# Kernel optimization log

Hardware: AMD Instinct MI355X
Metric: run time of the kernel (lower is better)

## Reference

```python
import jax, jax.numpy as jnp
import numpy as np

B, CIN, H, W = 32, 16, 32, 128
COUT = 128


def _run_direction(x_hwbc, p):
    # x_hwbc: (H, W, B, CIN); scan order is raster (top-to-bottom, left-to-right).
    # Predecessors: dim0 = cell above (previous row), dim1 = cell to the left.
    xi = jnp.einsum('hwbc,oc->hwbo', x_hwbc, p['w_ii'])
    xf = jnp.einsum('hwbc,oc->hwbo', x_hwbc, p['w_if'])
    xg = jnp.einsum('hwbc,oc->hwbo', x_hwbc, p['w_ig'])
    xo = jnp.einsum('hwbc,oc->hwbo', x_hwbc, p['w_io'])
    Wdim, Bdim = x_hwbc.shape[1], x_hwbc.shape[2]
    O = p['w_hi'].shape[0]
    ws0, ws1 = p['ws'][0], p['ws'][1]

    def branch(xi_, xf_, xg_, xo_, c, h):
        i = jax.nn.sigmoid(xi_ + h @ p['w_hi'].T + p['b_i'])
        f = jax.nn.sigmoid(xf_ + h @ p['w_hf'].T + p['b_f'])
        g = jnp.tanh(xg_ + h @ p['w_hg'].T + p['b_g'])
        o = jax.nn.sigmoid(xo_ + h @ p['w_ho'].T + p['b_o'])
        cn = f * c + i * g
        return cn, o * jnp.tanh(cn)

    def col_step(carry, inp):
        c_left, h_left = carry                      # (B, O)
        xi_, xf_, xg_, xo_, c_top, h_top = inp      # each (B, O)
        c0, h0 = branch(xi_, xf_, xg_, xo_, c_top, h_top)   # vertical predecessor
        c1, h1 = branch(xi_, xf_, xg_, xo_, c_left, h_left) # horizontal predecessor
        ct = ws0 * c0 + ws1 * c1 + p['bias']
        ht = ws0 * h0 + ws1 * h1 + p['bias']
        return (ct, ht), (ct, ht)

    def row_step(carry, row):
        c_top, h_top = carry                        # (W, B, O)
        xi_r, xf_r, xg_r, xo_r = row
        z = jnp.zeros((Bdim, O), xi_r.dtype)
        _, (c_row, h_row) = jax.lax.scan(col_step, (z, z), (xi_r, xf_r, xg_r, xo_r, c_top, h_top))
        return (c_row, h_row), h_row

    z_row = jnp.zeros((Wdim, Bdim, O), x_hwbc.dtype)
    _, h_all = jax.lax.scan(row_step, (z_row, z_row), (xi, xf, xg, xo))
    return h_all  # (H, W, B, O)


def _forward(x, w_ii, w_hi, b_i, w_if, w_hf, b_f, w_ig, w_hg, b_g,
             w_io, w_ho, b_o, weighted_sum, bias):
    # Four scan directions realized by flipping the grid (lr_tb, rl_tb, lr_bt, rl_bt).
    x_hwbc = jnp.transpose(x, (2, 3, 0, 1))  # (H, W, B, CIN)
    flips = [(False, False), (False, True), (True, False), (True, True)]
    outs = []
    for d, (fy, fx) in enumerate(flips):
        xd = x_hwbc
        if fy:
            xd = xd[::-1]
        if fx:
            xd = xd[:, ::-1]
        p = {'w_ii': w_ii[d], 'w_hi': w_hi[d], 'b_i': b_i[d],
             'w_if': w_if[d], 'w_hf': w_hf[d], 'b_f': b_f[d],
             'w_ig': w_ig[d], 'w_hg': w_hg[d], 'b_g': b_g[d],
             'w_io': w_io[d], 'w_ho': w_ho[d], 'b_o': b_o[d],
             'ws': weighted_sum[d], 'bias': bias[d]}
        h = _run_direction(xd, p)
        if fy:
            h = h[::-1]
        if fx:
            h = h[:, ::-1]
        outs.append(h)
    h4 = jnp.stack(outs)                      # (4, H, W, B, O)
    return jnp.transpose(h4, (0, 4, 3, 1, 2)) # (4, O, B, H, W)


def setup_inputs() -> dict:
    key = jax.random.key(0)
    ks = jax.random.split(key, 16)
    xw = lambda k: jax.random.normal(k, (4, COUT, CIN), jnp.float32) * 0.05
    hw = lambda k: jax.random.normal(k, (4, COUT, COUT), jnp.float32) * 0.05
    bb = lambda k: jax.random.normal(k, (4, COUT), jnp.float32) * 0.05
    return {
        'x': jax.random.normal(ks[0], (B, CIN, H, W), jnp.float32),
        'w_ii': xw(ks[1]), 'w_hi': hw(ks[2]), 'b_i': bb(ks[3]),
        'w_if': xw(ks[4]), 'w_hf': hw(ks[5]), 'b_f': bb(ks[6]),
        'w_ig': xw(ks[7]), 'w_hg': hw(ks[8]), 'b_g': bb(ks[9]),
        'w_io': xw(ks[10]), 'w_ho': hw(ks[11]), 'b_o': bb(ks[12]),
        'weighted_sum': jax.random.uniform(ks[13], (4, 2), jnp.float32),
        'bias': bb(ks[14]),
    }


def reference(x, w_ii, w_hi, b_i, w_if, w_hf, b_f, w_ig, w_hg, b_g,
              w_io, w_ho, b_o, weighted_sum, bias):
    return _forward(x, w_ii, w_hi, b_i, w_if, w_hf, b_f, w_ig, w_hg, b_g,
                    w_io, w_ho, b_o, weighted_sum, bias)
```

## Files before the change

### kernel.cpp

```cpp
#include <hip/hip_runtime.h>

#define Hh 32
#define Ww 128
#define BB 32
#define CC 16
#define OO 128
#define SPIN_CAP (1 << 23)
#define FSTRIDE 32

typedef __attribute__((ext_vector_type(8))) short short8;
typedef __attribute__((ext_vector_type(4))) float f32x4;

__device__ inline short f2bf(float f) {
    unsigned u = __builtin_bit_cast(unsigned, f);
    unsigned r = (u + 0x7FFFu + ((u >> 16) & 1u)) >> 16;
    return (short)r;
}
__device__ inline float bf2f(short s) {
    unsigned u = ((unsigned)(unsigned short)s) << 16;
    return __builtin_bit_cast(float, u);
}
__device__ inline float rcp_(float x) { return __builtin_amdgcn_rcpf(x); }
__device__ inline float sigm(float x) {
    return rcp_(1.f + __builtin_amdgcn_exp2f(-1.442695041f * x));
}
__device__ inline float tanh_(float x) {
    return 1.f - 2.f * rcp_(__builtin_amdgcn_exp2f(2.885390082f * x) + 1.f);
}

__device__ inline unsigned long long aload64(const unsigned long long* p) {
    return __hip_atomic_load(p, __ATOMIC_RELAXED, __HIP_MEMORY_SCOPE_AGENT);
}
__device__ inline void astore64(unsigned long long* p, unsigned long long v) {
    __hip_atomic_store(p, v, __ATOMIC_RELAXED, __HIP_MEMORY_SCOPE_AGENT);
}
__device__ inline void astore16(short* p, short v) {
    __hip_atomic_store(p, v, __ATOMIC_RELAXED, __HIP_MEMORY_SCOPE_AGENT);
}
__device__ inline int aloadI(const int* p) {
    return __hip_atomic_load(p, __ATOMIC_RELAXED, __HIP_MEMORY_SCOPE_AGENT);
}
__device__ inline void astoreI(int* p, int v) {
    __hip_atomic_store(p, v, __ATOMIC_RELAXED, __HIP_MEMORY_SCOPE_AGENT);
}

__global__ void mdlstm_init(const float* __restrict__ x, short* __restrict__ xT,
                            int* __restrict__ flags) {
    int idx = blockIdx.x * 256 + threadIdx.x;
    if (blockIdx.x < 64) flags[idx] = 0;
    int w = idx & 127;
    int h = (idx >> 7) & 31;
    int c = (idx >> 12) & 15;
    int b = idx >> 16;
    float v = x[idx];
    xT[((h * Ww + w) * BB + b) * CC + c] = f2bf(v);
}

__global__ void __launch_bounds__(512, 1) mdlstm_main(
    const short* __restrict__ xT,
    const float* __restrict__ w_ii, const float* __restrict__ w_hi, const float* __restrict__ b_i,
    const float* __restrict__ w_if, const float* __restrict__ w_hf, const float* __restrict__ b_f,
    const float* __restrict__ w_ig, const float* __restrict__ w_hg, const float* __restrict__ b_g,
    const float* __restrict__ w_io, const float* __restrict__ w_ho, const float* __restrict__ b_o,
    const float* __restrict__ wsum, const float* __restrict__ bias,
    short* __restrict__ hring, float* __restrict__ cring,
    int* __restrict__ prog, int* __restrict__ cons,
    float* __restrict__ out, int depth)
{
    const int chain = blockIdx.x & 7;
    const int r     = blockIdx.x >> 3;
    const int d     = chain >> 1;
    const int s     = chain & 1;
    const int b0    = s * 16;
    const bool fy   = (d >= 2);
    const bool fx   = (d & 1);
    const int hh    = fy ? (Hh - 1 - r) : r;

    const int tid  = threadIdx.x;
    const int wv   = tid >> 6;
    const int lane = tid & 63;
    const int lr   = lane & 15;
    const int lh   = lane >> 4;
    const int on   = wv * 16 + lr;

    __shared__ short stage[OO * 256];

    const float* whp[4] = {w_hi, w_hf, w_hg, w_ho};
    const float* wip[4] = {w_ii, w_if, w_ig, w_io};
    short8 whf[4][4];
    short8 wif_[4];
#pragma unroll
    for (int g = 0; g < 4; ++g) {
#pragma unroll
        for (int kt = 0; kt < 4; ++kt) {
            const float* p = whp[g] + ((d * OO + on) * OO + kt * 32 + lh * 8);
            short8 f;
#pragma unroll
            for (int j = 0; j < 8; ++j) f[j] = f2bf(p[j]);
            whf[g][kt] = f;
        }
        short8 fi = (short8)(short)0;
        if (lh < 2) {
            const float* p = wip[g] + ((d * OO + on) * CC + lh * 8);
#pragma unroll
            for (int j = 0; j < 8; ++j) fi[j] = f2bf(p[j]);
        }
        wif_[g] = fi;
    }

    const float bi  = b_i[d * OO + on];
    const float bf_ = b_f[d * OO + on];
    const float bg_ = b_g[d * OO + on];
    const float bo_ = b_o[d * OO + on];
    const float bb_ = bias[d * OO + on];
    const float ws0 = wsum[d * 2 + 0];
    const float ws1 = wsum[d * 2 + 1];

    int* topf      = prog + ((d * 32 + (r - 1)) * 2 + s) * FSTRIDE;
    int* myprog    = prog + ((d * 32 + r) * 2 + s) * FSTRIDE;
    int* mycons    = cons + ((d * 32 + r) * 2 + s) * FSTRIDE;
    int* consnext  = cons + ((d * 32 + (r + 1)) * 2 + s) * FSTRIDE;

    const int rbh_me  = ((d * 32 + r)     * 2 + s) * depth * (16 * OO);
    const int rbh_top = ((d * 32 + (r-1)) * 2 + s) * depth * (16 * OO);
    const int rbc_me  = ((d * 32 + r)     * 2 + s) * depth * (OO * 16);
    const int rbc_top = ((d * 32 + (r-1)) * 2 + s) * depth * (OO * 16);
    const int smask   = depth - 1;

    short8 hLf[4];
#pragma unroll
    for (int kt = 0; kt < 4; ++kt) hLf[kt] = (short8)(short)0;
    float cL[4] = {0.f, 0.f, 0.f, 0.f};

    short8 hTfB[4];
#pragma unroll
    for (int kt = 0; kt < 4; ++kt) hTfB[kt] = (short8)(short)0;
    float cTB[4] = {0.f, 0.f, 0.f, 0.f};

    int top_seen = 0, cons_seen = 0;
    const f32x4 zacc = {0.f, 0.f, 0.f, 0.f};

#pragma unroll 2
    for (int wsc = 0; wsc < Ww; ++wsc) {
        const int ww    = fx ? (Ww - 1 - wsc) : wsc;
        const int slot  = wsc & smask;
        const int wslot = ww & 15;
        const bool evenc = ((wsc & 1) == 0);

        short8 xf = (short8)(short)0;
        if (lh < 2) {
            const short8* p = (const short8*)(xT + ((hh * Ww + ww) * BB + b0 + lr) * CC + lh * 8);
            xf = __builtin_nontemporal_load(p);
        }

        short8 hTf[4];
        float cT[4];
        if (r > 0) {
            if (evenc) {
                const int need = wsc + 2;
                if (top_seen < need) {
                    int spin = 0;
                    while (top_seen < need && spin < SPIN_CAP) {
                        int v = 0;
                        if (lane == 0) v = aloadI(topf);
                        v = __shfl(v, 0, 64);
                        if (v < need) { __builtin_amdgcn_s_sleep(1); ++spin; } else top_seen = v;
                    }
                }
                const short* hb = hring + rbh_top + slot * (16 * OO) + lr * OO;
#pragma unroll
                for (int kt = 0; kt < 4; ++kt) {
                    union { unsigned long long q; short8 v8; } u, u2;
                    u.q = aload64((const unsigned long long*)(hb + kt * 32 + lh * 8));
                    (void)u2;
                    union { unsigned long long q[2]; short8 v; } w;
                    w.q[0] = aload64((const unsigned long long*)(hb + kt * 32 + lh * 8));
                    w.q[1] = aload64((const unsigned long long*)(hb + kt * 32 + lh * 8 + 4));
                    hTf[kt] = w.v;
                }
                const short* hb2 = hb + 16 * OO;
#pragma unroll
                for (int kt = 0; kt < 4; ++kt) {
                    union { unsigned long long q[2]; short8 v; } w;
                    w.q[0] = aload64((const unsigned long long*)(hb2 + kt * 32 + lh * 8));
                    w.q[1] = aload64((const unsigned long long*)(hb2 + kt * 32 + lh * 8 + 4));
                    hTfB[kt] = w.v;
                }
                const unsigned long long* cp =
                    (const unsigned long long*)(cring + rbc_top + slot * (OO * 16) + on * 16 + lh * 4);
                union { unsigned long long q; float f[2]; } c01, c23;
                c01.q = aload64(cp);
                c23.q = aload64(cp + 1);
                cT[0] = c01.f[0]; cT[1] = c01.f[1]; cT[2] = c23.f[0]; cT[3] = c23.f[1];
                const unsigned long long* cpB =
                    (const unsigned long long*)(cring + rbc_top + (slot + 1) * (OO * 16) + on * 16 + lh * 4);
                c01.q = aload64(cpB);
                c23.q = aload64(cpB + 1);
                cTB[0] = c01.f[0]; cTB[1] = c01.f[1]; cTB[2] = c23.f[0]; cTB[3] = c23.f[1];
            } else {
#pragma unroll
                for (int kt = 0; kt < 4; ++kt) hTf[kt] = hTfB[kt];
#pragma unroll
                for (int j = 0; j < 4; ++j) cT[j] = cTB[j];
            }
        } else {
#pragma unroll
            for (int kt = 0; kt < 4; ++kt) hTf[kt] = (short8)(short)0;
#pragma unroll
            for (int j = 0; j < 4; ++j) cT[j] = 0.f;
        }

        f32x4 ax[4], accL[4], accT[4];
#pragma unroll
        for (int g = 0; g < 4; ++g)
            ax[g] = __builtin_amdgcn_mfma_f32_16x16x32_bf16(xf, wif_[g], zacc, 0, 0, 0);
#pragma unroll
        for (int g = 0; g < 4; ++g) {
            f32x4 a = ax[g];
#pragma unroll
            for (int kt = 0; kt < 4; ++kt)
                a = __builtin_amdgcn_mfma_f32_16x16x32_bf16(hLf[kt], whf[g][kt], a, 0, 0, 0);
            accL[g] = a;
        }
#pragma unroll
        for (int g = 0; g < 4; ++g) {
            f32x4 a = ax[g];
#pragma unroll
            for (int kt = 0; kt < 4; ++kt)
                a = __builtin_amdgcn_mfma_f32_16x16x32_bf16(hTf[kt], whf[g][kt], a, 0, 0, 0);
            accT[g] = a;
        }

        float ctv[4];
        union { short sh[4]; unsigned long long q; } hpack;
#pragma unroll
        for (int j = 0; j < 4; ++j) {
            float iT = sigm(accT[0][j] + bi);
            float fT = sigm(accT[1][j] + bf_);
            float gT = tanh_(accT[2][j] + bg_);
            float oT = sigm(accT[3][j] + bo_);
            float c0 = fT * cT[j] + iT * gT;
            float h0 = oT * tanh_(c0);

            float iL = sigm(accL[0][j] + bi);
            float fL = sigm(accL[1][j] + bf_);
            float gL = tanh_(accL[2][j] + bg_);
            float oL = sigm(accL[3][j] + bo_);
            float c1 = fL * cL[j] + iL * gL;
            float h1 = oL * tanh_(c1);

            float ct = ws0 * c0 + ws1 * c1 + bb_;
            float ht = ws0 * h0 + ws1 * h1 + bb_;
            cL[j] = ct;
            ctv[j] = ct;
            hpack.sh[j] = f2bf(ht);
        }

        {
            const int g_on = (on >> 3) & 15;
            *(unsigned long long*)&stage[on * 256 + ((wslot ^ g_on) << 4) + lh * 4] = hpack.q;
        }

        if (r < 31 && evenc && wsc >= depth) {
            const int need = wsc - (depth - 2);
            if (cons_seen < need) {
                int spin = 0;
                while (cons_seen < need && spin < SPIN_CAP) {
                    int v = 0;
                    if (lane == 0) v = aloadI(consnext);
                    v = __shfl(v, 0, 64);
                    if (v < need) { __builtin_amdgcn_s_sleep(1); ++spin; } else cons_seen = v;
                }
            }
        }

        if (r < 31) {
            short* hp = hring + rbh_me + slot * (16 * OO) + on;
#pragma unroll
            for (int j = 0; j < 4; ++j)
                astore16(hp + (lh * 4 + j) * OO, hpack.sh[j]);
            union { float f[2]; unsigned long long q; } p01, p23;
            p01.f[0] = ctv[0]; p01.f[1] = ctv[1];
            p23.f[0] = ctv[2]; p23.f[1] = ctv[3];
            unsigned long long* cp =
                (unsigned long long*)(cring + rbc_me + slot * (OO * 16) + on * 16 + lh * 4);
            astore64(cp, p01.q);
            astore64(cp + 1, p23.q);
        }

        __syncthreads();

        if (!evenc && tid == 0) {
            if (r < 31) astoreI(myprog, wsc + 1);
            if (r > 0)  astoreI(mycons, wsc + 1);
        }

        if (r > 0 && !evenc && wsc < Ww - 1) {
            int v = 0;
            if (lane == 0) v = aloadI(topf);
            v = __shfl(v, 0, 64);
            if (v > top_seen) top_seen = v;
        }

#pragma unroll
        for (int kt = 0; kt < 4; ++kt) {
            const int col = ((wslot ^ (kt * 4 + lh)) << 4) + lr;
            short8 f;
#pragma unroll
            for (int jj = 0; jj < 8; ++jj)
                f[jj] = stage[(kt * 32 + lh * 8 + jj) * 256 + col];
            hLf[kt] = f;
        }

        if ((wsc & 15) == 15) {
            const int wbase = ww & ~15;
            const int q  = tid & 3;
            const int r0 = tid >> 2;
#pragma unroll
            for (int i = 0; i < 16; ++i) {
                const int row = r0 + (i << 7);
                const int o = row >> 4;
                const int b = row & 15;
                const int go = (o >> 3) & 15;
                f32x4 v;
#pragma unroll
                for (int k = 0; k < 4; ++k)
                    v[k] = bf2f(stage[o * 256 + (((q * 4 + k) ^ go) << 4) + b]);
                float* op = out + ((size_t)((d * OO + o) * BB + b0 + b)) * (Hh * Ww)
                                + hh * Ww + wbase + q * 4;
                __builtin_nontemporal_store(v, (f32x4*)op);
            }
            __syncthreads();
        }
    }
}

extern "C" void kernel_launch(void* const* d_in, const int* in_sizes, int n_in,
                              void* d_out, int out_size, void* d_ws, size_t ws_size,
                              hipStream_t stream) {
    (void)in_sizes; (void)n_in; (void)out_size;

    const float* x     = (const float*)d_in[0];
    const float* w_ii  = (const float*)d_in[1];
    const float* w_hi  = (const float*)d_in[2];
    const float* b_i   = (const float*)d_in[3];
    const float* w_if  = (const float*)d_in[4];
    const float* w_hf  = (const float*)d_in[5];
    const float* b_f   = (const float*)d_in[6];
    const float* w_ig  = (const float*)d_in[7];
    const float* w_hg  = (const float*)d_in[8];
    const float* b_g   = (const float*)d_in[9];
    const float* w_io  = (const float*)d_in[10];
    const float* w_ho  = (const float*)d_in[11];
    const float* b_o   = (const float*)d_in[12];
    const float* wsum  = (const float*)d_in[13];
    const float* bias  = (const float*)d_in[14];
    float* outp        = (float*)d_out;

    char* ws = (char*)d_ws;
    int*   flags  = (int*)ws;
    short* xTp    = (short*)(ws + (64u << 10));
    const size_t off_h = (64u << 10) + (4u << 20);

    int depth = 8;
    const size_t need8 = off_h + ((size_t)8 << 20) + ((size_t)16 << 20) + (1u << 20);
    if (ws_size < need8) depth = 4;

    short* hringp = (short*)(ws + off_h);
    float* cringp = (float*)(ws + off_h + ((size_t)depth << 20));
    int*   progp  = flags;
    int*   consp  = flags + 256 * FSTRIDE;

    hipLaunchKernelGGL(mdlstm_init, dim3(8192), dim3(256), 0, stream, x, xTp, flags);

    mdlstm_main<<<dim3(256), dim3(512), 0, stream>>>(
        xTp,
        w_ii, w_hi, b_i,
        w_if, w_hf, b_f,
        w_ig, w_hg, b_g,
        w_io, w_ho, b_o,
        wsum, bias,
        hringp, cringp, progp, consp,
        outp, depth);
}
```

Baseline: 1.249 ms.

## Prefetch next x column, simplify flag polling, defer flush barrier

Loads the input column for the next step during the current step's MFMA work, so the global load latency is hidden instead of stalling each step. Polling of the progress flags now has every lane read the flag directly, replacing the lane-0 load plus shuffle. The dead duplicate load in the top-row fetch is removed. The barrier after the 16-column output flush moves to just before the next write into the stage buffer, so the flush can overlap the next step's compute. The tradeoffs are more concurrent flag loads and one extra register vector live across the loop.

```diff
diff --git a/kernel.cpp b/kernel.cpp
--- a/kernel.cpp
+++ b/kernel.cpp
@@ -140,6 +140,13 @@
     int top_seen = 0, cons_seen = 0;
     const f32x4 zacc = {0.f, 0.f, 0.f, 0.f};
 
+    short8 xf_next = (short8)(short)0;
+    {
+        const int ww0 = fx ? (Ww - 1) : 0;
+        if (lh < 2)
+            xf_next = *(const short8*)(xT + ((hh * Ww + ww0) * BB + b0 + lr) * CC + lh * 8);
+    }
+
 #pragma unroll 2
     for (int wsc = 0; wsc < Ww; ++wsc) {
         const int ww    = fx ? (Ww - 1 - wsc) : wsc;
@@ -147,11 +154,7 @@
         const int wslot = ww & 15;
         const bool evenc = ((wsc & 1) == 0);
 
-        short8 xf = (short8)(short)0;
-        if (lh < 2) {
-            const short8* p = (const short8*)(xT + ((hh * Ww + ww) * BB + b0 + lr) * CC + lh * 8);
-            xf = __builtin_nontemporal_load(p);
-        }
+        const short8 xf = xf_next;
 
         short8 hTf[4];
         float cT[4];
@@ -161,18 +164,13 @@
                 if (top_seen < need) {
                     int spin = 0;
                     while (top_seen < need && spin < SPIN_CAP) {
-                        int v = 0;
-                        if (lane == 0) v = aloadI(topf);
-                        v = __shfl(v, 0, 64);
+                        const int v = aloadI(topf);
                         if (v < need) { __builtin_amdgcn_s_sleep(1); ++spin; } else top_seen = v;
                     }
                 }
                 const short* hb = hring + rbh_top + slot * (16 * OO) + lr * OO;
 #pragma unroll
                 for (int kt = 0; kt < 4; ++kt) {
-                    union { unsigned long long q; short8 v8; } u, u2;
-                    u.q = aload64((const unsigned long long*)(hb + kt * 32 + lh * 8));
-                    (void)u2;
                     union { unsigned long long q[2]; short8 v; } w;
                     w.q[0] = aload64((const unsigned long long*)(hb + kt * 32 + lh * 8));
                     w.q[1] = aload64((const unsigned long long*)(hb + kt * 32 + lh * 8 + 4));
@@ -222,6 +220,13 @@
                 a = __builtin_amdgcn_mfma_f32_16x16x32_bf16(hLf[kt], whf[g][kt], a, 0, 0, 0);
             accL[g] = a;
         }
+
+        if (wsc + 1 < Ww) {
+            const int wwN = fx ? (Ww - 2 - wsc) : (wsc + 1);
+            if (lh < 2)
+                xf_next = *(const short8*)(xT + ((hh * Ww + wwN) * BB + b0 + lr) * CC + lh * 8);
+        }
+
 #pragma unroll
         for (int g = 0; g < 4; ++g) {
             f32x4 a = ax[g];
@@ -256,6 +261,8 @@
             hpack.sh[j] = f2bf(ht);
         }
 
+        if ((wsc & 15) == 0 && wsc != 0) __syncthreads();
+
         {
             const int g_on = (on >> 3) & 15;
             *(unsigned long long*)&stage[on * 256 + ((wslot ^ g_on) << 4) + lh * 4] = hpack.q;
@@ -266,9 +273,7 @@
             if (cons_seen < need) {
                 int spin = 0;
                 while (cons_seen < need && spin < SPIN_CAP) {
-                    int v = 0;
-                    if (lane == 0) v = aloadI(consnext);
-                    v = __shfl(v, 0, 64);
+                    const int v = aloadI(consnext);
                     if (v < need) { __builtin_amdgcn_s_sleep(1); ++spin; } else cons_seen = v;
                 }
             }
@@ -296,9 +301,7 @@
         }
 
         if (r > 0 && !evenc && wsc < Ww - 1) {
-            int v = 0;
-            if (lane == 0) v = aloadI(topf);
-            v = __shfl(v, 0, 64);
+            const int v = aloadI(topf);
             if (v > top_seen) top_seen = v;
         }
 
@@ -330,7 +333,6 @@
                                 + hh * Ww + wbase + q * 4;
                 __builtin_nontemporal_store(v, (f32x4*)op);
             }
-            __syncthreads();
         }
     }
 }
```

Result: faster. 1.091 ms (-12.6%).
